# Kernel optimization log

Hardware: AMD Instinct MI355X
Metric: run time of the kernel (lower is better)

## Reference

```python
import jax, jax.numpy as jnp
import numpy as np

DIM = 1024
NUM_HEADS = 16
HEAD_D = DIM // NUM_HEADS


def setup_inputs() -> dict:
    key = jax.random.key(0)
    ks = jax.random.split(key, 9)
    s = 1.0 / np.sqrt(DIM)
    x = jax.random.normal(ks[0], (2, 2048, DIM), dtype=jnp.float32)
    Wq = jax.random.uniform(ks[1], (DIM, DIM), jnp.float32, -s, s)
    bq = jax.random.uniform(ks[2], (DIM,), jnp.float32, -s, s)
    Wk = jax.random.uniform(ks[3], (DIM, DIM), jnp.float32, -s, s)
    bk = jax.random.uniform(ks[4], (DIM,), jnp.float32, -s, s)
    Wv = jax.random.uniform(ks[5], (DIM, DIM), jnp.float32, -s, s)
    bv = jax.random.uniform(ks[6], (DIM,), jnp.float32, -s, s)
    Wo = jax.random.uniform(ks[7], (DIM, DIM), jnp.float32, -s, s)
    bo = jax.random.uniform(ks[8], (DIM,), jnp.float32, -s, s)
    return {"x": x, "Wq": Wq, "bq": bq, "Wk": Wk, "bk": bk,
            "Wv": Wv, "bv": bv, "Wo": Wo, "bo": bo}


def reference(x, Wq, bq, Wk, bk, Wv, bv, Wo, bo):
    B, T, D = x.shape
    H, Hd = NUM_HEADS, HEAD_D
    # torch Linear: x @ W.T + b
    q = (x @ Wq.T + bq).reshape(B, T, H, Hd).transpose(0, 2, 1, 3)  # [B,H,T,Hd]
    k = (x @ Wk.T + bk).reshape(B, T, H, Hd).transpose(0, 2, 1, 3)
    v = (x @ Wv.T + bv).reshape(B, T, H, Hd).transpose(0, 2, 1, 3)
    scores = jnp.einsum('bhqd,bhkd->bhqk', q, k) / jnp.sqrt(jnp.float32(Hd))
    causal = jnp.tril(jnp.ones((T, T), dtype=bool))  # [T,T]
    scores = jnp.where(causal[None, None], scores, -jnp.inf)
    probs = jax.nn.softmax(scores, axis=-1)
    ctx = jnp.einsum('bhqk,bhkd->bhqd', probs, v)
    out = ctx.transpose(0, 2, 1, 3).reshape(B, T, D)
    out = out @ Wo.T + bo
    return (out, (k, v))
```

## Files before the change

kernel.cpp:

```cpp
#include <hip/hip_runtime.h>

#define BB 2
#define TT 2048
#define DD 1024
#define HH 16
#define HD 64
#define MM (BB*TT)

typedef __bf16 bf16;
typedef __bf16 bf16x4 __attribute__((ext_vector_type(4)));
typedef __bf16 bf16x8 __attribute__((ext_vector_type(8)));
typedef float  f32x4  __attribute__((ext_vector_type(4)));

#define QSCALE 0.1803368801111244f
#define M0 16.0f

__device__ __forceinline__ void gl_lds16(const void* g, void* l) {
  __builtin_amdgcn_global_load_lds(
      (const __attribute__((address_space(1))) void*)g,
      (__attribute__((address_space(3))) void*)l, 16, 0, 0);
}
__device__ __forceinline__ f32x4 mfma16(bf16x8 a, bf16x8 b, f32x4 c) {
  return __builtin_amdgcn_mfma_f32_16x16x32_bf16(a, b, c, 0, 0, 0);
}

__global__ void cvt_f32_bf16(const float* __restrict__ src,
                             bf16* __restrict__ dst, int n4) {
  int i = blockIdx.x * blockDim.x + threadIdx.x;
  if (i < n4) {
    float4 v = ((const float4*)src)[i];
    bf16x4 o = { (bf16)v.x, (bf16)v.y, (bf16)v.z, (bf16)v.w };
    ((bf16x4*)dst)[i] = o;
  }
}
__global__ void cvt_w4(const float* __restrict__ s0, const float* __restrict__ s1,
                       const float* __restrict__ s2, const float* __restrict__ s3,
                       bf16* __restrict__ d0, bf16* __restrict__ d1,
                       bf16* __restrict__ d2, bf16* __restrict__ d3, int n4) {
  int i = blockIdx.x * blockDim.x + threadIdx.x;
  if (i >= n4) return;
  const float* s = (blockIdx.y == 0) ? s0 : (blockIdx.y == 1) ? s1 : (blockIdx.y == 2) ? s2 : s3;
  bf16*        d = (blockIdx.y == 0) ? d0 : (blockIdx.y == 1) ? d1 : (blockIdx.y == 2) ? d2 : d3;
  float4 v = ((const float4*)s)[i];
  bf16x4 o = { (bf16)v.x, (bf16)v.y, (bf16)v.z, (bf16)v.w };
  ((bf16x4*)d)[i] = o;
}

template<int BN>
__device__ __forceinline__ void tile_core(const bf16* __restrict__ A,
                                          const bf16* __restrict__ W,
                                          int m0, int n0,
                                          bf16* sA, bf16* sB, f32x4 acc[4][4]) {
  const int tid  = threadIdx.x;
  const int wv   = tid >> 6;
  const int l15  = tid & 15;
  const int quad = (tid & 63) >> 4;
  const int wy   = wv >> 1, wx = wv & 1;
  const int NF   = BN / 32;
  const int row  = tid >> 2;
  const int c8   = (tid & 3) * 8;
  const bf16* Ab = A + (size_t)(m0 + row) * DD + c8;
  const bf16* Wb = W + (size_t)(n0 + row) * DD + c8;
  char* lA = (char*)sA + wv * 1024;
  char* lB = (char*)sB + wv * 1024;
  for (int k0 = 0; k0 < DD; k0 += 32) {
    gl_lds16(Ab + k0,           lA);
    gl_lds16(Ab + 64 * DD + k0, lA + 4096);
    gl_lds16(Wb + k0,           lB);
    if (BN == 128) gl_lds16(Wb + 64 * DD + k0, lB + 4096);
    __syncthreads();
    bf16x8 af[4], bw[4];
    for (int mi = 0; mi < 4; mi++)
      af[mi] = *(const bf16x8*)(sA + (wy * 64 + mi * 16 + l15) * 32 + quad * 8);
    for (int ni = 0; ni < NF; ni++)
      bw[ni] = *(const bf16x8*)(sB + (wx * (BN / 2) + ni * 16 + l15) * 32 + quad * 8);
    for (int mi = 0; mi < 4; mi++)
      for (int ni = 0; ni < NF; ni++)
        acc[mi][ni] = mfma16(af[mi], bw[ni], acc[mi][ni]);
    __syncthreads();
  }
}

__launch_bounds__(256)
__global__ void gemm_qkv(const bf16* __restrict__ X,
                         const bf16* __restrict__ Wq, const bf16* __restrict__ Wk,
                         const bf16* __restrict__ Wv,
                         const float* __restrict__ bq, const float* __restrict__ bk,
                         const float* __restrict__ bv,
                         bf16* __restrict__ qb, bf16* __restrict__ kb,
                         bf16* __restrict__ vtb,
                         float* __restrict__ kf, float* __restrict__ vf) {
  __shared__ bf16 sA[128 * 32];
  __shared__ bf16 sB[128 * 32];
  const int bid = blockIdx.x;
  const int wv_ = threadIdx.x >> 6;
  const int l15 = threadIdx.x & 15, quad = (threadIdx.x & 63) >> 4;
  const int wy = wv_ >> 1, wx = wv_ & 1;
  if (bid < 512) {
    const int sel = bid >> 8;
    const bf16*  W    = sel ? Wk : Wq;
    const float* bias = sel ? bk : bq;
    const int m0 = ((bid & 255) >> 3) * 128;
    const int n0 = (bid & 7) * 128;
    f32x4 acc[4][4] = {};
    tile_core<128>(X, W, m0, n0, sA, sB, acc);
    for (int mi = 0; mi < 4; mi++)
      for (int ni = 0; ni < 4; ni++)
        for (int r = 0; r < 4; r++) {
          int m = m0 + wy * 64 + mi * 16 + quad * 4 + r;
          int n = n0 + wx * 64 + ni * 16 + l15;
          float v = acc[mi][ni][r] + bias[n];
          int b = m >> 11, t = m & (TT - 1);
          int h = n >> 6,  d = n & (HD - 1);
          size_t idx = ((size_t)(b * HH + h) * TT + t) * HD + d;
          if (sel == 0) qb[idx] = (bf16)(v * QSCALE);
          else { kb[idx] = (bf16)v; kf[idx] = v; }
        }
  } else {
    const int sub = bid - 512;
    const int m0 = (sub >> 6) * 128;
    const int n0 = (sub & 63) * 64;
    f32x4 acc[4][4] = {};
    tile_core<64>(Wv, X, m0, n0, sA, sB, acc);
    for (int mi = 0; mi < 4; mi++) {
      int mbase = m0 + wy * 64 + mi * 16 + quad * 4;
      float brv[4];
      for (int r = 0; r < 4; r++) brv[r] = bv[mbase + r];
      int h = mbase >> 6, dbase = mbase & (HD - 1);
      for (int ni = 0; ni < 2; ni++) {
        int tok = n0 + wx * 32 + ni * 16 + l15;
        int b = tok >> 11, t = tok & (TT - 1);
        int bh = b * HH + h;
        float4 vv;
        float* vp = &vv.x;
        for (int r = 0; r < 4; r++) {
          float v = acc[mi][ni][r] + brv[r];
          vp[r] = v;
          vtb[((size_t)bh * HD + dbase + r) * TT + t] = (bf16)v;
        }
        *(float4*)&vf[((size_t)bh * TT + t) * HD + dbase] = vv;
      }
    }
  }
}

__launch_bounds__(256)
__global__ void gemm_o(const bf16* __restrict__ A, const bf16* __restrict__ W,
                       const float* __restrict__ bias, float* __restrict__ out) {
  __shared__ bf16 sA[128 * 32];
  __shared__ bf16 sB[64 * 32];
  const int m0 = blockIdx.x * 128;
  const int n0 = blockIdx.y * 64;
  f32x4 acc[4][4] = {};
  tile_core<64>(A, W, m0, n0, sA, sB, acc);
  const int wv = threadIdx.x >> 6;
  const int l15 = threadIdx.x & 15, quad = (threadIdx.x & 63) >> 4;
  const int wy = wv >> 1, wx = wv & 1;
  for (int mi = 0; mi < 4; mi++)
    for (int ni = 0; ni < 2; ni++)
      for (int r = 0; r < 4; r++) {
        int m = m0 + wy * 64 + mi * 16 + quad * 4 + r;
        int n = n0 + wx * 32 + ni * 16 + l15;
        out[(size_t)m * DD + n] = acc[mi][ni][r] + bias[n];
      }
}

__launch_bounds__(256, 4)
__global__ void attn_fwd(const bf16* __restrict__ Q, const bf16* __restrict__ Kg,
                         const bf16* __restrict__ Vt, bf16* __restrict__ ctx) {
  __shared__ __align__(16) bf16 kbuf[2][4096];
  __shared__ __align__(16) bf16 vbuf[2][4096];
  __shared__ __align__(16) bf16 pbuf[4][1024];
  const int tid  = threadIdx.x;
  const int lane = tid & 63, wv = tid >> 6;
  const int quad = lane >> 4, l15 = lane & 15;
  const int bx = blockIdx.x;
  const int sl = bx >> 3;
  const int c  = 31 - (sl >> 2);
  const int bh = (bx & 7) + 8 * (sl & 3);
  const int qr = c * 64 + wv * 16;
  const int ntiles = c + 1;

  const bf16* Kbh = Kg + (size_t)bh * TT * HD;
  const bf16* Vbh = Vt + (size_t)bh * HD * TT;

  const int k0s = tid >> 3,            c0s = (tid & 7) ^ (k0s & 7);
  const int s1  = 256 + tid;
  const int k1s = s1 >> 3,             c1s = (s1 & 7) ^ (k1s & 7);

  int foff[4][2];
  for (int sub = 0; sub < 4; sub++)
    for (int h = 0; h < 2; h++)
      foff[sub][h] = (((sub * 16 + l15) * 8) + ((h * 4 + quad) ^ (l15 & 7))) * 8;

  const bf16* qp = Q + ((size_t)bh * TT + qr + l15) * HD + quad * 8;
  bf16x8 aq0 = *(const bf16x8*)qp;
  bf16x8 aq1 = *(const bf16x8*)(qp + 32);

  float lrow = 0.f;
  f32x4 acc[4] = {};
  bf16* pb = pbuf[wv];
  const int pswz = l15 & 7;

  gl_lds16(Kbh + (size_t)k0s * HD + c0s * 8, (char*)kbuf[0] + wv * 1024);
  gl_lds16(Kbh + (size_t)k1s * HD + c1s * 8, (char*)kbuf[0] + 4096 + wv * 1024);
  gl_lds16(Vbh + (size_t)k0s * TT + c0s * 8, (char*)vbuf[0] + wv * 1024);
  gl_lds16(Vbh + (size_t)k1s * TT + c1s * 8, (char*)vbuf[0] + 4096 + wv * 1024);

  for (int t = 0; t < ntiles; t++) {
    const int kt = t * 64;
    __syncthreads();
    if (t + 1 < ntiles) {
      bf16* kn = kbuf[(t + 1) & 1];
      bf16* vn = vbuf[(t + 1) & 1];
      gl_lds16(Kbh + (size_t)(kt + 64 + k0s) * HD + c0s * 8, (char*)kn + wv * 1024);
      gl_lds16(Kbh + (size_t)(kt + 64 + k1s) * HD + c1s * 8, (char*)kn + 4096 + wv * 1024);
      gl_lds16(Vbh + (size_t)k0s * TT + kt + 64 + c0s * 8, (char*)vn + wv * 1024);
      gl_lds16(Vbh + (size_t)k1s * TT + kt + 64 + c1s * 8, (char*)vn + 4096 + wv * 1024);
    }
    const bf16* kc = kbuf[t & 1];
    const bf16* vc = vbuf[t & 1];
    const bool last = (t == ntiles - 1);

    float p[4][4];
    for (int sub = 0; sub < 4; sub++) {
      if (last && kt + sub * 16 > qr + 15) {
        p[sub][0] = p[sub][1] = p[sub][2] = p[sub][3] = 0.f;
        continue;
      }
      bf16x8 ak0 = *(const bf16x8*)(kc + foff[sub][0]);
      bf16x8 ak1 = *(const bf16x8*)(kc + foff[sub][1]);
      f32x4 z = {};
      f32x4 st = mfma16(ak0, aq0, z);
      st = mfma16(ak1, aq1, st);
      if (last) {
        for (int r = 0; r < 4; r++) {
          int k_abs = kt + sub * 16 + quad * 4 + r;
          p[sub][r] = (k_abs > qr + l15) ? 0.f
                      : __builtin_amdgcn_exp2f(st[r] - M0);
        }
      } else {
        for (int r = 0; r < 4; r++)
          p[sub][r] = __builtin_amdgcn_exp2f(st[r] - M0);
      }
      lrow += (p[sub][0] + p[sub][1]) + (p[sub][2] + p[sub][3]);
    }

    for (int sub = 0; sub < 4; sub++) {
      bf16x4 pk = { (bf16)p[sub][0], (bf16)p[sub][1], (bf16)p[sub][2], (bf16)p[sub][3] };
      int cch = sub * 2 + (quad >> 1);
      *(bf16x4*)&pb[l15 * 64 + ((cch ^ pswz) * 8 + (quad & 1) * 4)] = pk;
    }
    bf16x8 ap0 = *(const bf16x8*)&pb[l15 * 64 + ((quad ^ pswz) * 8)];
    bf16x8 ap1 = *(const bf16x8*)&pb[l15 * 64 + (((4 + quad) ^ pswz) * 8)];

    for (int ni = 0; ni < 4; ni++) {
      bf16x8 v0 = *(const bf16x8*)(vc + foff[ni][0]);
      bf16x8 v1 = *(const bf16x8*)(vc + foff[ni][1]);
      acc[ni] = mfma16(ap0, v0, acc[ni]);
      acc[ni] = mfma16(ap1, v1, acc[ni]);
    }
  }

  lrow += __shfl_xor(lrow, 16, 64);
  lrow += __shfl_xor(lrow, 32, 64);
  float invl = 1.f / lrow;
  float invq[4];
  for (int r = 0; r < 4; r++)
    invq[r] = __shfl(invl, (lane & 48) | (quad * 4 + r), 64);
  int b = bh >> 4, h = bh & (HH - 1);
  for (int ni = 0; ni < 4; ni++)
    for (int r = 0; r < 4; r++) {
      int tq = qr + quad * 4 + r;
      ctx[((size_t)(b * TT + tq)) * DD + h * HD + ni * 16 + l15] = (bf16)(acc[ni][r] * invq[r]);
    }
}

extern "C" void kernel_launch(void* const* d_in, const int* in_sizes, int n_in,
                              void* d_out, int out_size, void* d_ws, size_t ws_size,
                              hipStream_t stream) {
  const float* x  = (const float*)d_in[0];
  const float* Wq = (const float*)d_in[1];
  const float* bq = (const float*)d_in[2];
  const float* Wk = (const float*)d_in[3];
  const float* bk = (const float*)d_in[4];
  const float* Wv = (const float*)d_in[5];
  const float* bv = (const float*)d_in[6];
  const float* Wo = (const float*)d_in[7];
  const float* bo = (const float*)d_in[8];
  float* out = (float*)d_out;
  float* outK = out + (size_t)MM * DD;
  float* outV = out + (size_t)2 * MM * DD;

  char* ws = (char*)d_ws;
  bf16* xb   = (bf16*)(ws);
  bf16* wqb  = (bf16*)(ws + (8  << 20));
  bf16* wkb  = (bf16*)(ws + (10 << 20));
  bf16* wvb  = (bf16*)(ws + (12 << 20));
  bf16* wob  = (bf16*)(ws + (14 << 20));
  bf16* qbuf = (bf16*)(ws + (16 << 20));
  bf16* kbuf = (bf16*)(ws + (24 << 20));
  bf16* vtb  = (bf16*)(ws + (32 << 20));
  bf16* ctxb = (bf16*)(ws + (40 << 20));

  cvt_f32_bf16<<<MM * DD / 4 / 256, 256, 0, stream>>>(x, xb, MM * DD / 4);
  cvt_w4<<<dim3(DD * DD / 4 / 256, 4), 256, 0, stream>>>(Wq, Wk, Wv, Wo, wqb, wkb, wvb, wob, DD * DD / 4);

  gemm_qkv<<<1024, 256, 0, stream>>>(xb, wqb, wkb, wvb, bq, bk, bv,
                                     qbuf, kbuf, vtb, outK, outV);

  attn_fwd<<<1024, 256, 0, stream>>>(qbuf, kbuf, vtb, ctxb);

  gemm_o<<<dim3(MM / 128, DD / 64), 256, 0, stream>>>(ctxb, wob, bo, out);
}
```

Before: 199.3 us.

## Swizzle GEMM LDS tiles, merge conversion kernels, enlarge V-projection tiles

The x and weight fp32-to-bf16 conversions are merged into one launch, saving a kernel launch. The GEMM shared-memory tiles get an XOR swizzle on the 16-byte column chunk, meant to cut LDS bank conflicts on the MFMA fragment reads. The V-projection part of gemm_qkv moves from 128x64 to 128x128 tiles, so the grid shrinks from 1024 to 768 blocks. Fewer, larger blocks raise reuse but lower parallelism in that phase.

```diff
diff --git a/kernel.cpp b/kernel.cpp
--- a/kernel.cpp
+++ b/kernel.cpp
@@ -24,26 +24,26 @@
   return __builtin_amdgcn_mfma_f32_16x16x32_bf16(a, b, c, 0, 0, 0);
 }
 
-__global__ void cvt_f32_bf16(const float* __restrict__ src,
-                             bf16* __restrict__ dst, int n4) {
+__global__ void cvt_all(const float* __restrict__ x,
+                        const float* __restrict__ w0, const float* __restrict__ w1,
+                        const float* __restrict__ w2, const float* __restrict__ w3,
+                        bf16* __restrict__ xd,
+                        bf16* __restrict__ d0, bf16* __restrict__ d1,
+                        bf16* __restrict__ d2, bf16* __restrict__ d3) {
   int i = blockIdx.x * blockDim.x + threadIdx.x;
-  if (i < n4) {
-    float4 v = ((const float4*)src)[i];
-    bf16x4 o = { (bf16)v.x, (bf16)v.y, (bf16)v.z, (bf16)v.w };
-    ((bf16x4*)dst)[i] = o;
+  const float* s;
+  bf16* d;
+  int off;
+  if (i < (1 << 20)) { s = x; d = xd; off = i; }
+  else {
+    int j = (i - (1 << 20)) >> 18;
+    off = (i - (1 << 20)) & ((1 << 18) - 1);
+    s = (j == 0) ? w0 : (j == 1) ? w1 : (j == 2) ? w2 : w3;
+    d = (j == 0) ? d0 : (j == 1) ? d1 : (j == 2) ? d2 : d3;
   }
-}
-__global__ void cvt_w4(const float* __restrict__ s0, const float* __restrict__ s1,
-                       const float* __restrict__ s2, const float* __restrict__ s3,
-                       bf16* __restrict__ d0, bf16* __restrict__ d1,
-                       bf16* __restrict__ d2, bf16* __restrict__ d3, int n4) {
-  int i = blockIdx.x * blockDim.x + threadIdx.x;
-  if (i >= n4) return;
-  const float* s = (blockIdx.y == 0) ? s0 : (blockIdx.y == 1) ? s1 : (blockIdx.y == 2) ? s2 : s3;
-  bf16*        d = (blockIdx.y == 0) ? d0 : (blockIdx.y == 1) ? d1 : (blockIdx.y == 2) ? d2 : d3;
-  float4 v = ((const float4*)s)[i];
+  float4 v = ((const float4*)s)[off];
   bf16x4 o = { (bf16)v.x, (bf16)v.y, (bf16)v.z, (bf16)v.w };
-  ((bf16x4*)d)[i] = o;
+  ((bf16x4*)d)[off] = o;
 }
 
 template<int BN>
@@ -58,9 +58,10 @@
   const int wy   = wv >> 1, wx = wv & 1;
   const int NF   = BN / 32;
   const int row  = tid >> 2;
-  const int c8   = (tid & 3) * 8;
-  const bf16* Ab = A + (size_t)(m0 + row) * DD + c8;
-  const bf16* Wb = W + (size_t)(n0 + row) * DD + c8;
+  const int cc   = (tid & 3) ^ ((row >> 1) & 3);
+  const int swz  = (l15 >> 1) & 3;
+  const bf16* Ab = A + (size_t)(m0 + row) * DD + cc * 8;
+  const bf16* Wb = W + (size_t)(n0 + row) * DD + cc * 8;
   char* lA = (char*)sA + wv * 1024;
   char* lB = (char*)sB + wv * 1024;
   for (int k0 = 0; k0 < DD; k0 += 32) {
@@ -71,9 +72,9 @@
     __syncthreads();
     bf16x8 af[4], bw[4];
     for (int mi = 0; mi < 4; mi++)
-      af[mi] = *(const bf16x8*)(sA + (wy * 64 + mi * 16 + l15) * 32 + quad * 8);
+      af[mi] = *(const bf16x8*)(sA + (wy * 64 + mi * 16 + l15) * 32 + (quad ^ swz) * 8);
     for (int ni = 0; ni < NF; ni++)
-      bw[ni] = *(const bf16x8*)(sB + (wx * (BN / 2) + ni * 16 + l15) * 32 + quad * 8);
+      bw[ni] = *(const bf16x8*)(sB + (wx * (BN / 2) + ni * 16 + l15) * 32 + (quad ^ swz) * 8);
     for (int mi = 0; mi < 4; mi++)
       for (int ni = 0; ni < NF; ni++)
         acc[mi][ni] = mfma16(af[mi], bw[ni], acc[mi][ni]);
@@ -118,17 +119,17 @@
         }
   } else {
     const int sub = bid - 512;
-    const int m0 = (sub >> 6) * 128;
-    const int n0 = (sub & 63) * 64;
+    const int m0 = (sub >> 5) * 128;
+    const int n0 = (sub & 31) * 128;
     f32x4 acc[4][4] = {};
-    tile_core<64>(Wv, X, m0, n0, sA, sB, acc);
+    tile_core<128>(Wv, X, m0, n0, sA, sB, acc);
     for (int mi = 0; mi < 4; mi++) {
       int mbase = m0 + wy * 64 + mi * 16 + quad * 4;
       float brv[4];
       for (int r = 0; r < 4; r++) brv[r] = bv[mbase + r];
       int h = mbase >> 6, dbase = mbase & (HD - 1);
-      for (int ni = 0; ni < 2; ni++) {
-        int tok = n0 + wx * 32 + ni * 16 + l15;
+      for (int ni = 0; ni < 4; ni++) {
+        int tok = n0 + wx * 64 + ni * 16 + l15;
         int b = tok >> 11, t = tok & (TT - 1);
         int bh = b * HH + h;
         float4 vv;
@@ -184,9 +185,9 @@
   const bf16* Kbh = Kg + (size_t)bh * TT * HD;
   const bf16* Vbh = Vt + (size_t)bh * HD * TT;
 
-  const int k0s = tid >> 3,            c0s = (tid & 7) ^ (k0s & 7);
+  const int k0s = tid >> 3,  c0s = (tid & 7) ^ (k0s & 7);
   const int s1  = 256 + tid;
-  const int k1s = s1 >> 3,             c1s = (s1 & 7) ^ (k1s & 7);
+  const int k1s = s1 >> 3,   c1s = (s1 & 7) ^ (k1s & 7);
 
   int foff[4][2];
   for (int sub = 0; sub < 4; sub++)
@@ -303,11 +304,11 @@
   bf16* vtb  = (bf16*)(ws + (32 << 20));
   bf16* ctxb = (bf16*)(ws + (40 << 20));
 
-  cvt_f32_bf16<<<MM * DD / 4 / 256, 256, 0, stream>>>(x, xb, MM * DD / 4);
-  cvt_w4<<<dim3(DD * DD / 4 / 256, 4), 256, 0, stream>>>(Wq, Wk, Wv, Wo, wqb, wkb, wvb, wob, DD * DD / 4);
-
-  gemm_qkv<<<1024, 256, 0, stream>>>(xb, wqb, wkb, wvb, bq, bk, bv,
-                                     qbuf, kbuf, vtb, outK, outV);
+  cvt_all<<<(2 << 20) / 256, 256, 0, stream>>>(x, Wq, Wk, Wv, Wo,
+                                               xb, wqb, wkb, wvb, wob);
+
+  gemm_qkv<<<768, 256, 0, stream>>>(xb, wqb, wkb, wvb, bq, bk, bv,
+                                    qbuf, kbuf, vtb, outK, outV);
 
   attn_fwd<<<1024, 256, 0, stream>>>(qbuf, kbuf, vtb, ctxb);
 
```

Result: no change. 198.8 us (-0.3%).
